# Kernel optimization log

Hardware: AMD Instinct MI355X
Metric: run time of the kernel (lower is better)

## Reference

```python
import jax, jax.numpy as jnp
import numpy as np

N = 100000
E = 1600000
D_IN = 64
D_OUT = 64
LN_EPS = 1e-5


def setup_inputs() -> dict:
    key = jax.random.key(0)
    k1, k2, k3 = jax.random.split(key, 3)
    x = jax.random.normal(k1, (N, D_IN), dtype=jnp.float32)
    edge_index = jax.random.randint(k2, (2, E), 0, N, dtype=jnp.int64)
    # nn.Linear(in_dim*2, out_dim): weight [out, 2*in], bias [out]
    W = jax.random.normal(k3, (D_OUT, 2 * D_IN), dtype=jnp.float32) * (1.0 / np.sqrt(2 * D_IN))
    b = jnp.zeros((D_OUT,), dtype=jnp.float32)
    gamma = jnp.ones((D_OUT,), dtype=jnp.float32)
    beta = jnp.zeros((D_OUT,), dtype=jnp.float32)
    return {"x": x, "edge_index": edge_index, "W": W, "b": b, "gamma": gamma, "beta": beta}


def reference(x, edge_index, W, b, gamma, beta):
    i, j = edge_index[0], edge_index[1]          # dst, src
    msg = x[j]                                    # [E, D] gather of source features
    agg = jax.ops.segment_sum(msg, i, num_segments=N)                      # [N, D]
    deg = jax.ops.segment_sum(jnp.ones((E,), x.dtype), i, num_segments=N)  # [N]
    agg = agg / jnp.maximum(deg, 1.0)[:, None]    # mean aggregation
    h = jnp.concatenate([x, agg], axis=-1)        # [N, 2D]
    out = jax.nn.relu(h @ W.T + b)                # [N, D_OUT]
    # LayerNorm over last dim (dropout p=0 -> identity)
    mu = jnp.mean(out, axis=-1, keepdims=True)
    var = jnp.var(out, axis=-1, keepdims=True)
    return (out - mu) * jax.lax.rsqrt(var + LN_EPS) * gamma + beta
```

## Files before the change

### kernel.cpp

```cpp
#include <hip/hip_runtime.h>

#define LN_EPS 1e-5f
#define SBSH   14
#define NSB    7
#define CAP1   268288
#define CPS    131
#define BN     128
#define BC     2368
#define NBK    782
#define CSTRIDE 8

typedef __attribute__((ext_vector_type(8))) short short8;
typedef __attribute__((ext_vector_type(8))) unsigned short ushort8;
typedef __attribute__((ext_vector_type(4))) float v4f;

__device__ __forceinline__ unsigned short f2bf(float f) {
    union { float f; unsigned u; } v; v.f = f;
    unsigned r = (v.u + 0x7fffu + ((v.u >> 16) & 1u)) >> 16;
    return (unsigned short)r;
}
__device__ __forceinline__ float bf2f(unsigned short h) {
    union { unsigned u; float f; } v; v.u = ((unsigned)h) << 16;
    return v.f;
}

__global__ __launch_bounds__(256) void bin1_kernel(
    const int* __restrict__ ei, int* __restrict__ cursor1,
    int* __restrict__ pairs1, const float* __restrict__ W,
    unsigned short* __restrict__ WTB, const float4* __restrict__ x4,
    ushort4* __restrict__ xb4, int E, int N)
{
    __shared__ int h[8], hbase[8];
    int t = threadIdx.x;

    if (blockIdx.x == 0) {
        for (int i = t; i < 8192; i += 256) {
            int j = i & 7, l = (i >> 3) & 63, st = i >> 9;
            int s = st >> 2, tt = st & 3;
            WTB[i] = f2bf(W[(tt * 16 + (l & 15)) * 128 + s * 32 + (l >> 4) * 8 + j]);
        }
    }
    {
        int total4 = N * 16;
        for (int i = blockIdx.x * 256 + t; i < total4; i += gridDim.x * 256) {
            float4 v = x4[i];
            ushort4 u;
            u.x = f2bf(v.x); u.y = f2bf(v.y); u.z = f2bf(v.z); u.w = f2bf(v.w);
            xb4[i] = u;
        }
    }

    if (t < 8) h[t] = 0;
    __syncthreads();
    int e0 = blockIdx.x * 2048;
    int dstA[8], srcA[8], rkA[8];
    #pragma unroll
    for (int i = 0; i < 8; ++i) {
        int e = e0 + i * 256 + t;
        int dst = 0, src = 0, rk = -1;
        if (e < E) {
            dst = ei[e]; src = ei[E + e];
            if ((unsigned)dst < (unsigned)N) {
                rk = atomicAdd(&h[dst >> SBSH], 1);
                if ((unsigned)src >= (unsigned)N) src = 0;
            } else { dst = 0; }
        }
        dstA[i] = dst; srcA[i] = src; rkA[i] = rk;
    }
    __syncthreads();
    if (t < 8) {
        int c = h[t];
        hbase[t] = c ? atomicAdd(&cursor1[t * 16], c) : 0;
    }
    __syncthreads();
    #pragma unroll
    for (int i = 0; i < 8; ++i) {
        if (rkA[i] >= 0) {
            int sb = dstA[i] >> SBSH;
            int slot = hbase[sb] + rkA[i];
            if (slot < CAP1)
                pairs1[(size_t)sb * CAP1 + slot] = ((dstA[i] & 16383) << 17) | srcA[i];
        }
    }
}

__global__ __launch_bounds__(256) void bin2_kernel(
    const int* __restrict__ cursor1, const int* __restrict__ pairs1,
    int* __restrict__ cursor2, int* __restrict__ pairs2)
{
    __shared__ int h[128], hbase[128];
    int t = threadIdx.x;
    int sb = blockIdx.x / CPS;
    int off0 = (blockIdx.x % CPS) * 2048;
    int tot = cursor1[sb * 16]; if (tot > CAP1) tot = CAP1;
    int m = tot - off0;
    if (m <= 0) return;
    if (m > 2048) m = 2048;
    if (t < 128) h[t] = 0;
    __syncthreads();
    const int* p1 = pairs1 + (size_t)sb * CAP1 + off0;
    int pvA[8], rkA[8];
    #pragma unroll
    for (int i = 0; i < 8; ++i) {
        int idx = i * 256 + t;
        int pv = 0, rk = -1;
        if (idx < m) { pv = p1[idx]; rk = atomicAdd(&h[(pv >> 24) & 127], 1); }
        pvA[i] = pv; rkA[i] = rk;
    }
    __syncthreads();
    if (t < 128) {
        int c = h[t];
        hbase[t] = c ? atomicAdd(&cursor2[(sb * 128 + t) * CSTRIDE], c) : 0;
    }
    __syncthreads();
    #pragma unroll
    for (int i = 0; i < 8; ++i) {
        if (rkA[i] >= 0) {
            int bl = (pvA[i] >> 24) & 127;
            int g = sb * 128 + bl;
            int slot = hbase[bl] + rkA[i];
            if (g < NBK && slot < BC)
                pairs2[(size_t)g * BC + slot] = pvA[i] & 0xFFFFFF;
        }
    }
}

__global__ __launch_bounds__(1024, 8) void sortgather_kernel(
    const int* __restrict__ cursor2, const int* __restrict__ pairs2,
    const unsigned short* __restrict__ xb, unsigned short* __restrict__ aggb, int N)
{
    __shared__ int srcS[BC];
    __shared__ int cnt[BN], off[BN], cur[BN];
    int t = threadIdx.x;
    int g = blockIdx.x;
    int bsize = cursor2[g * CSTRIDE]; if (bsize > BC) bsize = BC;
    const int* pb = pairs2 + (size_t)g * BC;

    if (t < BN) cnt[t] = 0;
    __syncthreads();
    for (int i = t; i < bsize; i += 1024) atomicAdd(&cnt[(pb[i] >> 17) & 127], 1);
    __syncthreads();
    if (t < BN) off[t] = cnt[t];
    __syncthreads();
    for (int s = 1; s < BN; s <<= 1) {
        int v = (t < BN && t >= s) ? off[t - s] : 0;
        __syncthreads();
        if (t < BN) off[t] += v;
        __syncthreads();
    }
    if (t < BN) { int ex = off[t] - cnt[t]; off[t] = ex; cur[t] = ex; }
    __syncthreads();
    for (int i = t; i < bsize; i += 1024) {
        int p = pb[i];
        int pos = atomicAdd(&cur[(p >> 17) & 127], 1);
        srcS[pos] = p & 0x1FFFF;
    }
    __syncthreads();

    int lane = t & 63, wv = t >> 6;
    int g8 = lane >> 3, f8 = lane & 7;
    for (int u = 0; u < 8; ++u) {
        int ln = wv * 8 + u;
        int deg = cnt[ln], base = off[ln];
        float acc[8];
        #pragma unroll
        for (int k = 0; k < 8; ++k) acc[k] = 0.f;
        for (int jb = 0; jb < deg; jb += 64) {
            int m = deg - jb; if (m > 64) m = 64;
            int idx = (lane < m) ? srcS[base + jb + lane] : 0;
            for (int j = 0; j < m; j += 16) {
                int n0 = __shfl(idx, (j + g8) & 63);
                int n1 = __shfl(idx, (j + 8 + g8) & 63);
                float w0 = (j + g8 < m) ? 1.f : 0.f;
                float w1 = (j + 8 + g8 < m) ? 1.f : 0.f;
                short8 a0 = *(const short8*)(xb + (size_t)n0 * 64 + f8 * 8);
                short8 a1 = *(const short8*)(xb + (size_t)n1 * 64 + f8 * 8);
                #pragma unroll
                for (int k = 0; k < 8; ++k)
                    acc[k] = fmaf(w0, bf2f((unsigned short)a0[k]), acc[k]);
                #pragma unroll
                for (int k = 0; k < 8; ++k)
                    acc[k] = fmaf(w1, bf2f((unsigned short)a1[k]), acc[k]);
            }
        }
        #pragma unroll
        for (int k = 0; k < 8; ++k) {
            acc[k] += __shfl_xor(acc[k], 8);
            acc[k] += __shfl_xor(acc[k], 16);
            acc[k] += __shfl_xor(acc[k], 32);
        }
        int node = g * BN + ln;
        if (lane < 8 && node < N) {
            float inv = 1.0f / fmaxf((float)deg, 1.0f);
            ushort8 r;
            #pragma unroll
            for (int k = 0; k < 8; ++k) r[k] = f2bf(acc[k] * inv);
            *(ushort8*)(aggb + (size_t)node * 64 + lane * 8) = r;
        }
    }
}

__global__ __launch_bounds__(256) void linear_kernel(
    const unsigned short* __restrict__ xb, const unsigned short* __restrict__ aggb,
    const unsigned short* __restrict__ WTB, const float* __restrict__ b,
    const float* __restrict__ gamma, const float* __restrict__ beta,
    float* __restrict__ out, int N)
{
    int lane = threadIdx.x & 63;
    int wv   = threadIdx.x >> 6;
    int nb   = blockIdx.x * 64 + wv * 16;
    if (nb >= N) return;
    int c = lane & 15, q = lane >> 4;
    int nm = nb + c; if (nm >= N) nm = N - 1;

    short8 bf[4][4];
    const short8* WB = (const short8*)WTB;
    #pragma unroll
    for (int s = 0; s < 4; ++s)
        #pragma unroll
        for (int tt = 0; tt < 4; ++tt)
            bf[s][tt] = WB[(s * 4 + tt) * 64 + lane];

    v4f acc[4];
    #pragma unroll
    for (int tt = 0; tt < 4; ++tt) acc[tt] = 0.f;

    #pragma unroll
    for (int s = 0; s < 2; ++s) {
        short8 af = *(const short8*)(xb + (size_t)nm * 64 + s * 32 + q * 8);
        #pragma unroll
        for (int tt = 0; tt < 4; ++tt)
            acc[tt] = __builtin_amdgcn_mfma_f32_16x16x32_bf16(af, bf[s][tt], acc[tt], 0, 0, 0);
    }
    #pragma unroll
    for (int s = 0; s < 2; ++s) {
        short8 af = *(const short8*)(aggb + (size_t)nm * 64 + s * 32 + q * 8);
        #pragma unroll
        for (int tt = 0; tt < 4; ++tt)
            acc[tt] = __builtin_amdgcn_mfma_f32_16x16x32_bf16(af, bf[2 + s][tt], acc[tt], 0, 0, 0);
    }

    float bb[4], gg[4], be[4];
    #pragma unroll
    for (int tt = 0; tt < 4; ++tt) {
        bb[tt] = b[tt * 16 + c];
        gg[tt] = gamma[tt * 16 + c];
        be[tt] = beta[tt * 16 + c];
    }
    #pragma unroll
    for (int r = 0; r < 4; ++r) {
        int node = nb + q * 4 + r;
        float v[4]; float s0 = 0.f, q0 = 0.f;
        #pragma unroll
        for (int tt = 0; tt < 4; ++tt) {
            float vv = acc[tt][r] + bb[tt];
            vv = fmaxf(vv, 0.f);
            v[tt] = vv; s0 += vv; q0 += vv * vv;
        }
        #pragma unroll
        for (int o = 1; o <= 8; o <<= 1) {
            s0 += __shfl_xor(s0, o);
            q0 += __shfl_xor(q0, o);
        }
        float mu  = s0 * (1.0f / 64.0f);
        float var = q0 * (1.0f / 64.0f) - mu * mu;
        float rs  = rsqrtf(var + LN_EPS);
        if (node < N) {
            #pragma unroll
            for (int tt = 0; tt < 4; ++tt)
                out[(size_t)node * 64 + tt * 16 + c] = (v[tt] - mu) * rs * gg[tt] + be[tt];
        }
    }
}

extern "C" void kernel_launch(void* const* d_in, const int* in_sizes, int n_in,
                              void* d_out, int out_size, void* d_ws, size_t ws_size,
                              hipStream_t stream)
{
    const float* x     = (const float*)d_in[0];
    const int*   ei    = (const int*)d_in[1];
    const float* W     = (const float*)d_in[2];
    const float* b     = (const float*)d_in[3];
    const float* gamma = (const float*)d_in[4];
    const float* beta  = (const float*)d_in[5];

    int N = in_sizes[0] / 64;
    int E = in_sizes[1] / 2;

    int* wsI = (int*)d_ws;
    int* cursor1 = wsI;
    int* cursor2 = wsI + 128;
    unsigned short* WTB = (unsigned short*)(wsI + 128 + 896 * CSTRIDE);
    int* pairs2 = wsI + 128 + 896 * CSTRIDE + 4096;
    unsigned short* xb = (unsigned short*)(pairs2 + (size_t)NBK * BC);

    int* pairs1 = (int*)d_out;
    unsigned short* aggb = (unsigned short*)d_in[1];

    float* out = (float*)d_out;

    hipMemsetAsync(cursor1, 0, (size_t)(128 + 896 * CSTRIDE) * sizeof(int), stream);

    int b1 = (E + 2047) / 2048;
    bin1_kernel<<<b1, 256, 0, stream>>>(ei, cursor1, pairs1, W, WTB,
                                        (const float4*)x, (ushort4*)xb, E, N);

    bin2_kernel<<<NSB * CPS, 256, 0, stream>>>(cursor1, pairs1, cursor2, pairs2);

    sortgather_kernel<<<NBK, 1024, 0, stream>>>(cursor2, pairs2, xb, aggb, N);

    int lb = (N + 63) / 64;
    linear_kernel<<<lb, 256, 0, stream>>>(xb, aggb, WTB, b, gamma, beta, out, N);
}
```

Before: 185.0 us.

## Privatize bin1 histograms, double edges per block, remap gather to node-per-8-lanes

bin1 now handles 4096 edges per block and keeps 8 private copies of the superbucket histogram, selected by thread index, so fewer lanes contend on each LDS atomic. Per-copy bases are computed by a small prefix over the copies. sortgather now assigns each 8-lane group its own destination node and walks that node's neighbour list directly, with no shuffles, masks or cross-lane reduction. Lanes in a wave now loop for different degrees, so divergence grows, but per-neighbour overhead drops. The launch-bounds occupancy hint on sortgather was also removed.

```diff
diff --git a/kernel.cpp b/kernel.cpp
--- a/kernel.cpp
+++ b/kernel.cpp
@@ -30,8 +30,10 @@
     unsigned short* __restrict__ WTB, const float4* __restrict__ x4,
     ushort4* __restrict__ xb4, int E, int N)
 {
-    __shared__ int h[8], hbase[8];
+    __shared__ int h[64];
+    __shared__ int hbase[64];
     int t = threadIdx.x;
+    int cp = t & 7;
 
     if (blockIdx.x == 0) {
         for (int i = t; i < 8192; i += 256) {
@@ -50,18 +52,18 @@
         }
     }
 
-    if (t < 8) h[t] = 0;
-    __syncthreads();
-    int e0 = blockIdx.x * 2048;
-    int dstA[8], srcA[8], rkA[8];
-    #pragma unroll
-    for (int i = 0; i < 8; ++i) {
+    for (int i = t; i < 64; i += 256) h[i] = 0;
+    __syncthreads();
+    int e0 = blockIdx.x * 4096;
+    int dstA[16], srcA[16], rkA[16];
+    #pragma unroll
+    for (int i = 0; i < 16; ++i) {
         int e = e0 + i * 256 + t;
         int dst = 0, src = 0, rk = -1;
         if (e < E) {
             dst = ei[e]; src = ei[E + e];
             if ((unsigned)dst < (unsigned)N) {
-                rk = atomicAdd(&h[dst >> SBSH], 1);
+                rk = atomicAdd(&h[cp * 8 + (dst >> SBSH)], 1);
                 if ((unsigned)src >= (unsigned)N) src = 0;
             } else { dst = 0; }
         }
@@ -69,15 +71,20 @@
     }
     __syncthreads();
     if (t < 8) {
-        int c = h[t];
-        hbase[t] = c ? atomicAdd(&cursor1[t * 16], c) : 0;
-    }
-    __syncthreads();
-    #pragma unroll
-    for (int i = 0; i < 8; ++i) {
+        int tot = 0;
+        #pragma unroll
+        for (int c = 0; c < 8; ++c) tot += h[c * 8 + t];
+        int gb = tot ? atomicAdd(&cursor1[t * 16], tot) : 0;
+        int run = gb;
+        #pragma unroll
+        for (int c = 0; c < 8; ++c) { hbase[c * 8 + t] = run; run += h[c * 8 + t]; }
+    }
+    __syncthreads();
+    #pragma unroll
+    for (int i = 0; i < 16; ++i) {
         if (rkA[i] >= 0) {
             int sb = dstA[i] >> SBSH;
-            int slot = hbase[sb] + rkA[i];
+            int slot = hbase[cp * 8 + sb] + rkA[i];
             if (slot < CAP1)
                 pairs1[(size_t)sb * CAP1 + slot] = ((dstA[i] & 16383) << 17) | srcA[i];
         }
@@ -125,7 +132,7 @@
     }
 }
 
-__global__ __launch_bounds__(1024, 8) void sortgather_kernel(
+__global__ __launch_bounds__(1024) void sortgather_kernel(
     const int* __restrict__ cursor2, const int* __restrict__ pairs2,
     const unsigned short* __restrict__ xb, unsigned short* __restrict__ aggb, int N)
 {
@@ -159,44 +166,38 @@
 
     int lane = t & 63, wv = t >> 6;
     int g8 = lane >> 3, f8 = lane & 7;
-    for (int u = 0; u < 8; ++u) {
-        int ln = wv * 8 + u;
-        int deg = cnt[ln], base = off[ln];
-        float acc[8];
-        #pragma unroll
-        for (int k = 0; k < 8; ++k) acc[k] = 0.f;
-        for (int jb = 0; jb < deg; jb += 64) {
-            int m = deg - jb; if (m > 64) m = 64;
-            int idx = (lane < m) ? srcS[base + jb + lane] : 0;
-            for (int j = 0; j < m; j += 16) {
-                int n0 = __shfl(idx, (j + g8) & 63);
-                int n1 = __shfl(idx, (j + 8 + g8) & 63);
-                float w0 = (j + g8 < m) ? 1.f : 0.f;
-                float w1 = (j + 8 + g8 < m) ? 1.f : 0.f;
-                short8 a0 = *(const short8*)(xb + (size_t)n0 * 64 + f8 * 8);
-                short8 a1 = *(const short8*)(xb + (size_t)n1 * 64 + f8 * 8);
-                #pragma unroll
-                for (int k = 0; k < 8; ++k)
-                    acc[k] = fmaf(w0, bf2f((unsigned short)a0[k]), acc[k]);
-                #pragma unroll
-                for (int k = 0; k < 8; ++k)
-                    acc[k] = fmaf(w1, bf2f((unsigned short)a1[k]), acc[k]);
-            }
-        }
-        #pragma unroll
-        for (int k = 0; k < 8; ++k) {
-            acc[k] += __shfl_xor(acc[k], 8);
-            acc[k] += __shfl_xor(acc[k], 16);
-            acc[k] += __shfl_xor(acc[k], 32);
-        }
-        int node = g * BN + ln;
-        if (lane < 8 && node < N) {
-            float inv = 1.0f / fmaxf((float)deg, 1.0f);
-            ushort8 r;
-            #pragma unroll
-            for (int k = 0; k < 8; ++k) r[k] = f2bf(acc[k] * inv);
-            *(ushort8*)(aggb + (size_t)node * 64 + lane * 8) = r;
-        }
+    int ln = wv * 8 + g8;
+    int deg = cnt[ln], base = off[ln];
+
+    float acc[8];
+    #pragma unroll
+    for (int k = 0; k < 8; ++k) acc[k] = 0.f;
+
+    int j = 0;
+    for (; j + 2 <= deg; j += 2) {
+        int s0 = srcS[base + j];
+        int s1 = srcS[base + j + 1];
+        short8 a0 = *(const short8*)(xb + (size_t)s0 * 64 + f8 * 8);
+        short8 a1 = *(const short8*)(xb + (size_t)s1 * 64 + f8 * 8);
+        #pragma unroll
+        for (int k = 0; k < 8; ++k) acc[k] += bf2f((unsigned short)a0[k]);
+        #pragma unroll
+        for (int k = 0; k < 8; ++k) acc[k] += bf2f((unsigned short)a1[k]);
+    }
+    if (j < deg) {
+        int s0 = srcS[base + j];
+        short8 a0 = *(const short8*)(xb + (size_t)s0 * 64 + f8 * 8);
+        #pragma unroll
+        for (int k = 0; k < 8; ++k) acc[k] += bf2f((unsigned short)a0[k]);
+    }
+
+    int node = g * BN + ln;
+    if (node < N) {
+        float inv = 1.0f / fmaxf((float)deg, 1.0f);
+        ushort8 r;
+        #pragma unroll
+        for (int k = 0; k < 8; ++k) r[k] = f2bf(acc[k] * inv);
+        *(ushort8*)(aggb + (size_t)node * 64 + f8 * 8) = r;
     }
 }
 
@@ -301,7 +302,7 @@
 
     hipMemsetAsync(cursor1, 0, (size_t)(128 + 896 * CSTRIDE) * sizeof(int), stream);
 
-    int b1 = (E + 2047) / 2048;
+    int b1 = (E + 4095) / 4096;
     bin1_kernel<<<b1, 256, 0, stream>>>(ei, cursor1, pairs1, W, WTB,
                                         (const float4*)x, (ushort4*)xb, E, N);
 
```

New measurement: 168.2 us. -9.1%, faster.
